# Optimization experiments

Hardware: AMD Instinct MI355X
Metric: run time of the kernel (lower is better)

Reference implementation:

```python
import jax, jax.numpy as jnp
import numpy as np
import math

N, C, T, V = 8, 256, 128, 25
H, HC = 8, 32            # num_heads, head_channels
W, DIL = 3, 1            # window, dilation
O = 256                  # out_channels
PAD = (W + (W - 1) * (DIL - 1) - 1) // 2
B, L = N * T, W * V


def _ln(x, g, b):
    m = jnp.mean(x, -1, keepdims=True)
    v = jnp.var(x, -1, keepdims=True)
    return (x - m) * jax.lax.rsqrt(v + 1e-5) * g + b


def setup_inputs() -> dict:
    key = jax.random.key(0)
    ks = iter(jax.random.split(key, 40))
    def w(shape):
        return jax.random.normal(next(ks), shape, jnp.float32) * 0.02
    d = {"x": jax.random.normal(next(ks), (N, C, T, V), jnp.float32)}
    d.update(
        ln1_g=jnp.ones((C,)), ln1_b=jnp.zeros((C,)),
        Wq=w((C, C)), bq=jnp.zeros((C,)), Wqa=w((C, H)), bqa=jnp.zeros((H,)),
        Wk=w((C, C)), bk=jnp.zeros((C,)), Wka=w((C, H)), bka=jnp.zeros((H,)),
        Wv=w((C, C)), bv=jnp.zeros((C,)), Wt=w((C, C)), bt=jnp.zeros((C,)),
        Wp=w((C, C)), bp=jnp.zeros((C,)),
        ffn_g=jnp.ones((C,)), ffn_b=jnp.zeros((C,)),
        W1=w((C, C)), b1=jnp.zeros((C,)), W2=w((C, C)), b2=jnp.zeros((C,)),
        tn_g=jnp.ones((C,)), tn_b=jnp.zeros((C,)),
        c1_w=w((C, O)), c1_b=jnp.zeros((O,)),
        c2_w=w((W, O, O)), c2_b=jnp.zeros((O,)),
    )
    return d


def reference(x, ln1_g, ln1_b, Wq, bq, Wqa, bqa, Wk, bk, Wka, bka, Wv, bv,
              Wt, bt, Wp, bp, ffn_g, ffn_b, W1, b1, W2, b2, tn_g, tn_b,
              c1_w, c1_b, c2_w, c2_b):
    scale = 1.0 / math.sqrt(HC)
    # ---- Unfold over time: build window of frames around each t (nn.Unfold) ----
    xp = jnp.pad(x, ((0, 0), (0, 0), (PAD, PAD), (0, 0)))
    win = jnp.stack([jax.lax.dynamic_slice_in_dim(xp, k * DIL, T, 2) for k in range(W)], 2)  # (N,C,W,T,V)
    seq = win.transpose(0, 3, 2, 4, 1).reshape(B, L, C)  # (N*T, W*V, C)

    sep = lambda z: z.reshape(B, L, H, HC).transpose(0, 2, 1, 3)  # (B,H,L,HC)
    grp = lambda z: z.transpose(0, 2, 1, 3).reshape(B, -1, C)

    # ---- SpatioTemporalAttention (eval: dropouts off) ----
    nx = _ln(seq, ln1_g, ln1_b)
    q = nx @ Wq + bq                                            # (B,L,C)
    qw = jax.nn.softmax((q @ Wqa + bqa).transpose(0, 2, 1) * scale, axis=-1)  # (B,H,L)
    pq = jnp.einsum('bhl,bhlc->bhc', qw, sep(q)).reshape(B, 1, C)             # pooled query
    keys = nx @ Wk + bk
    kw = jax.nn.softmax(((keys * pq) @ Wka + bka).transpose(0, 2, 1) * scale, axis=-1)
    pk = jnp.einsum('bhl,bhlc->bhc', kw, sep(keys))             # pooled key (B,H,HC)
    vals = sep(nx @ Wv + bv)
    kv = grp(vals * pk[:, :, None, :]) @ Wt + bt                # (B,L,C)
    attn = (kv + q) @ Wp + bp                                   # residual-in-heads == plain add

    # ---- AttentionBranch residual + FFN ----
    att = attn + seq
    f = _ln(att, ffn_g, ffn_b)
    y = jax.nn.gelu(f @ W1 + b1, approximate=False) @ W2 + b2 + att  # (B,L,C)

    # ---- temporal branch: LN -> regroup frames -> 1x1 conv -> GELU -> (W,1) conv stride W ----
    t5 = _ln(y, tn_g, tn_b).reshape(N, T, W, V, C)
    h = jax.nn.gelu(t5 @ c1_w + c1_b, approximate=False)        # (N,T,W,V,O)
    out = jnp.einsum('ntwvi,wio->ntvo', h, c2_w) + c2_b         # stride==kernel conv == window contraction
    return out.transpose(0, 3, 1, 2)                            # (N,O,T,V)
```

## Files before the change

### kernel.cpp

```cpp
#include <hip/hip_runtime.h>


#define DI __device__ __forceinline__

constexpr int CC   = 256;
constexpr int CL   = 75;
constexpr int CV   = 25;
constexpr int CT   = 128;
constexpr int TP   = 130;
constexpr int MPAD = 8 * TP * CV;
constexpr int MBL  = 1024 * CL;
constexpr int MOUT = 8 * CT * CV;
constexpr float SM_SCALE = 0.17677669529663687f;

typedef __bf16 bf16x8 __attribute__((ext_vector_type(8)));
typedef float f32x4 __attribute__((ext_vector_type(4)));

DI float bf2f(unsigned short u) { return __uint_as_float(((unsigned)u) << 16); }
DI float bf2f_lo(unsigned u) { return __uint_as_float(u << 16); }
DI float bf2f_hi(unsigned u) { return __uint_as_float(u & 0xffff0000u); }
DI unsigned short f2bf(float f) {
  unsigned u = __float_as_uint(f);
  u += 0x7fffu + ((u >> 16) & 1u);
  return (unsigned short)(u >> 16);
}
DI unsigned packbf(float a, float b) {
  return (unsigned)f2bf(a) | ((unsigned)f2bf(b) << 16);
}
DI float geluf(float x) { return 0.5f * x * (1.f + erff(x * 0.70710678118654752440f)); }

DI void gll16(const unsigned short* g, unsigned short* l) {
  __builtin_amdgcn_global_load_lds(
      (const __attribute__((address_space(1))) unsigned int*)g,
      (__attribute__((address_space(3))) unsigned int*)l, 16, 0, 0);
}

DI int arow(int r) {
  int b = r / CL;
  int l = r - b * CL;
  int w = l / CV;
  int v = l - w * CV;
  int t = b & (CT - 1);
  int n = b >> 7;
  return (n * TP + t + w) * CV + v;
}

__global__ __launch_bounds__(256) void k_transpose(const float* __restrict__ x,
                                                   unsigned short* __restrict__ xtp) {
  __shared__ float tile[32][33];
  const int n = blockIdx.z;
  const int c0 = blockIdx.x * 32;
  const int tv0 = blockIdx.y * 32;
  const int tx = threadIdx.x & 31, ty = threadIdx.x >> 5;
#pragma unroll
  for (int j = 0; j < 32; j += 8) {
    tile[ty + j][tx] = x[((size_t)(n * CC + c0 + ty + j)) * 3200 + tv0 + tx];
  }
  __syncthreads();
#pragma unroll
  for (int j = 0; j < 32; j += 8) {
    int tv = tv0 + ty + j;
    int st = tv / CV, v = tv - st * CV;
    size_t row = ((size_t)n * TP + st + 1) * CV + v;
    xtp[row * CC + c0 + tx] = f2bf(tile[tx][ty + j]);
  }
}

__global__ __launch_bounds__(256) void k_zero_pad(unsigned short* __restrict__ xtp) {
  int i = blockIdx.x * 256 + threadIdx.x;
  int c = i & 255;
  int rid = i >> 8;
  int n = rid / 50;
  int rem = rid - n * 50;
  int side = rem / 25;
  int v = rem - side * 25;
  size_t row = ((size_t)n * TP + side * (TP - 1)) * CV + v;
  xtp[row * CC + c] = 0;
}

struct TJobs {
  const float* src[10];
  unsigned short* dst[10];
  int stride[10];
  int off[10];
};
__global__ __launch_bounds__(256) void k_wtrans(TJobs J) {
  __shared__ float tile[32][33];
  const int j = blockIdx.z;
  const float* src = J.src[j];
  unsigned short* dst = J.dst[j];
  const int stride = J.stride[j], off = J.off[j];
  const int k0 = blockIdx.x * 32, n0 = blockIdx.y * 32;
  const int tx = threadIdx.x & 31, ty = threadIdx.x >> 5;
#pragma unroll
  for (int jj = 0; jj < 32; jj += 8)
    tile[ty + jj][tx] = src[(size_t)(k0 + ty + jj) * 256 + n0 + tx];
  __syncthreads();
#pragma unroll
  for (int jj = 0; jj < 32; jj += 8)
    dst[(size_t)(n0 + ty + jj) * stride + off + k0 + tx] = f2bf(tile[tx][ty + jj]);
}

__global__ __launch_bounds__(256) void k_wtwp(const float* __restrict__ Wt,
                                              const float* __restrict__ Wp,
                                              unsigned short* __restrict__ fused) {
  __shared__ float wrow[256];
  const int k = blockIdx.x, n = threadIdx.x;
  wrow[n] = Wt[(size_t)k * 256 + n];
  __syncthreads();
  float acc = 0.f;
  for (int j = 0; j < 256; ++j) acc = fmaf(wrow[j], Wp[(size_t)j * 256 + n], acc);
  fused[(size_t)n * 512 + k] = f2bf(acc);
}

__global__ __launch_bounds__(256) void k_bias2(const float* __restrict__ bt,
                                               const float* __restrict__ Wp,
                                               const float* __restrict__ bp,
                                               const float* __restrict__ bq,
                                               const float* __restrict__ bk,
                                               const float* __restrict__ bv,
                                               float* __restrict__ bias2,
                                               float* __restrict__ bias3) {
  const int n = threadIdx.x;
  float acc = bp[n];
  for (int j = 0; j < 256; ++j) acc = fmaf(bt[j], Wp[(size_t)j * 256 + n], acc);
  bias2[n] = acc;
  bias3[n] = bq[n];
  bias3[256 + n] = bk[n];
  bias3[512 + n] = bv[n];
}

__global__ __launch_bounds__(256) void k_ln4(const unsigned short* __restrict__ X,
                                             const float* __restrict__ g,
                                             const float* __restrict__ b,
                                             unsigned short* __restrict__ Y) {
  const int row = blockIdx.x * 4 + (threadIdx.x >> 6);
  const int lane = threadIdx.x & 63;
  const uint2 u = *(const uint2*)(X + (size_t)row * CC + lane * 4);
  const float x0 = bf2f_lo(u.x), x1 = bf2f_hi(u.x), x2 = bf2f_lo(u.y), x3 = bf2f_hi(u.y);
  float s = x0 + x1 + x2 + x3;
  float q = x0 * x0 + x1 * x1 + x2 * x2 + x3 * x3;
#pragma unroll
  for (int o = 32; o; o >>= 1) { s += __shfl_xor(s, o); q += __shfl_xor(q, o); }
  const float mean = s * (1.f / CC);
  const float var = q * (1.f / CC) - mean * mean;
  const float rs = rsqrtf(var + 1e-5f);
  const float4 g4 = *(const float4*)(g + lane * 4);
  const float4 b4 = *(const float4*)(b + lane * 4);
  uint2 o2;
  o2.x = packbf((x0 - mean) * rs * g4.x + b4.x, (x1 - mean) * rs * g4.y + b4.y);
  o2.y = packbf((x2 - mean) * rs * g4.z + b4.z, (x3 - mean) * rs * g4.w + b4.w);
  *(uint2*)(Y + (size_t)row * CC + lane * 4) = o2;
}

template <int AMODE, int EPI, int KD, bool MULTI>
__global__ __launch_bounds__(512) void k_mgemm(const unsigned short* __restrict__ A,
                                               const unsigned short* __restrict__ BwT,
                                               const float* __restrict__ bias,
                                               unsigned short* __restrict__ Cout,
                                               float* __restrict__ FOut,
                                               int M) {
  if constexpr (MULTI) {
    const int z = blockIdx.y;
    BwT += (size_t)z * (256 * 256);
    bias += z * 256;
    Cout += (size_t)z * MPAD * CC;
  }
  __shared__ unsigned short SH[20480];
  const int tid = threadIdx.x;
  const int lane = tid & 63;
  const int wid = tid >> 6;
  const int wm = wid >> 2, wn = wid & 3;
  const int r0 = blockIdx.x * 64;
  f32x4 acc[2][4] = {};

  const bool sa = tid < 256;
  const int rA = r0 + (tid >> 2);
  const int seg8 = (tid & 3) * 8;
  const bool valid = sa && (rA < M);
  int hrb = 0;
  if (valid && AMODE == 4) {
    const int nb = rA / 3200, rr = rA - nb * 3200;
    const int tq = rr / 25, vq = rr - tq * 25;
    hrb = (nb * CT + tq) * CL + vq;
  }

  auto loadA4 = [&](int k0) -> uint4 {
    uint4 u = make_uint4(0, 0, 0, 0);
    if (!valid) return u;
    const int w = k0 >> 8;
    u = *(const uint4*)(A + (size_t)(hrb + w * CV) * CC + (k0 & 255) + seg8);
    return u;
  };
  auto stageB = [&](int buf, int k0) {
    unsigned short* bs = SH + 4096 + buf * 8192;
#pragma unroll
    for (int pp = 0; pp < 2; ++pp) {
      const int s = tid + pp * 512;
      gll16(BwT + (size_t)(s >> 2) * KD + k0 + (s & 3) * 8, bs + s * 8);
    }
  };
  auto stageAg = [&](int buf, int k0) {
    if (valid) gll16(A + (size_t)rA * CC + k0 + seg8, SH + buf * 2048 + tid * 8);
  };

  stageB(0, 0);
  if constexpr (AMODE == 0) {
    stageAg(0, 0);
  } else {
    const uint4 a0 = loadA4(0);
    if (sa) *(uint4*)(SH + tid * 8) = a0;
  }
  __syncthreads();

  constexpr int NT = KD / 32;
  int cur = 0;
  for (int t = 0; t < NT; ++t) {
    const int nxt = cur ^ 1;
    const bool more = (t + 1 < NT);
    uint4 an;
    if (more) {
      stageB(nxt, (t + 1) * 32);
      if constexpr (AMODE == 0) stageAg(nxt, (t + 1) * 32);
      else an = loadA4((t + 1) * 32);
    }
    const unsigned short* as = SH + cur * 2048;
    const unsigned short* bs = SH + 4096 + cur * 8192;
    bf16x8 af[2], bfr[4];
#pragma unroll
    for (int mi = 0; mi < 2; ++mi)
      af[mi] = *(const bf16x8*)(as + (wm * 32 + mi * 16 + (lane & 15)) * 32 + (lane >> 4) * 8);
#pragma unroll
    for (int ni = 0; ni < 4; ++ni)
      bfr[ni] = *(const bf16x8*)(bs + (wn * 64 + ni * 16 + (lane & 15)) * 32 + (lane >> 4) * 8);
#pragma unroll
    for (int mi = 0; mi < 2; ++mi)
#pragma unroll
      for (int ni = 0; ni < 4; ++ni)
        acc[mi][ni] = __builtin_amdgcn_mfma_f32_16x16x32_bf16(af[mi], bfr[ni], acc[mi][ni], 0, 0, 0);
    if (more) {
      if constexpr (AMODE != 0) {
        if (sa) *(uint4*)(SH + nxt * 2048 + tid * 8) = an;
      }
      __syncthreads();
      cur = nxt;
    }
  }

  const int ln15 = lane & 15, lq = lane >> 4;
  if constexpr (EPI == 4) {
#pragma unroll
    for (int mi = 0; mi < 2; ++mi) {
#pragma unroll
      for (int ni = 0; ni < 4; ++ni) {
        const int col = wn * 64 + ni * 16 + ln15;
        const float bcol = bias[col];
        const int rbase = r0 + wm * 32 + mi * 16 + lq * 4;
        const int nb = rbase / 3200, rr = rbase - nb * 3200;
        float4 v;
        v.x = acc[mi][ni][0] + bcol;
        v.y = acc[mi][ni][1] + bcol;
        v.z = acc[mi][ni][2] + bcol;
        v.w = acc[mi][ni][3] + bcol;
        *(float4*)(FOut + (size_t)nb * 819200 + (size_t)col * 3200 + rr) = v;
      }
    }
  } else {
    constexpr int LDC = 260;
    __syncthreads();
#pragma unroll
    for (int mi = 0; mi < 2; ++mi) {
#pragma unroll
      for (int ni = 0; ni < 4; ++ni) {
        const int col = wn * 64 + ni * 16 + ln15;
        const float bcol = bias[col];
#pragma unroll
        for (int rg = 0; rg < 4; ++rg) {
          const int lrow = wm * 32 + mi * 16 + lq * 4 + rg;
          SH[lrow * LDC + col] = f2bf(acc[mi][ni][rg] + bcol);
        }
      }
    }
    __syncthreads();
#pragma unroll
    for (int i = 0; i < 4; ++i) {
      const int idx = tid + i * 512;
      const int row = idx >> 5, ch = idx & 31;
      const int gr = r0 + row;
      if (gr < M)
        *(uint4*)(Cout + (size_t)gr * CC + ch * 8) = *(const uint4*)&SH[row * LDC + ch * 8];
    }
  }
}

__global__ __launch_bounds__(512, 4) void k_chain(
    const unsigned short* __restrict__ VP, const unsigned short* __restrict__ QP,
    const float* __restrict__ PK, const unsigned short* __restrict__ XTP,
    const unsigned short* __restrict__ fusedB, const float* __restrict__ bias2,
    const unsigned short* __restrict__ W1T, const float* __restrict__ b1,
    const unsigned short* __restrict__ W2T, const float* __restrict__ b2,
    const float* __restrict__ ffn_g, const float* __restrict__ ffn_b,
    const unsigned short* __restrict__ c1wT, const float* __restrict__ c1b,
    const float* __restrict__ tn_g, const float* __restrict__ tn_b,
    unsigned short* __restrict__ Hout) {
  constexpr int LDC = 264;
  __shared__ unsigned short SH[16896 + 4096 + 16384];
  unsigned short* ACT = SH;
  unsigned short* AS = SH + 16896;
  unsigned short* BS = SH + 16896 + 4096;
  const int tid = threadIdx.x;
  const int lane = tid & 63, wid = tid >> 6;
  const int wm = wid >> 2, wn = wid & 3;
  const int ln15 = lane & 15, lq = lane >> 4;
  const int r0 = blockIdx.x * 64;

  const bool sa = tid < 256;
  const int rA = r0 + (tid >> 2);
  const int seg8 = (tid & 3) * 8;
  int ar = 0, bb = 0;
  if (sa) { ar = arow(rA); bb = rA / CL; }
  int xrow[8];
#pragma unroll
  for (int i = 0; i < 8; ++i)
    xrow[i] = arow(r0 + wm * 32 + (i >> 2) * 16 + lq * 4 + (i & 3));

  auto stageB = [&](const unsigned short* BwT, int KD, int buf, int k0) {
    unsigned short* bs = BS + buf * 8192;
#pragma unroll
    for (int pp = 0; pp < 2; ++pp) {
      const int s = tid + pp * 512;
      gll16(BwT + (size_t)(s >> 2) * KD + k0 + (s & 3) * 8, bs + s * 8);
    }
  };
  auto loadA5 = [&](int k0) -> uint4 {
    uint4 u = make_uint4(0, 0, 0, 0);
    if (!sa) return u;
    if (k0 < 256) {
      const int kg = k0 + seg8;
      const uint4 t4 = *(const uint4*)(VP + (size_t)ar * CC + kg);
      const float* sv = PK + bb * CC + kg;
      const float4 s0 = *(const float4*)sv;
      const float4 s1 = *(const float4*)(sv + 4);
      u.x = packbf(bf2f_lo(t4.x) * s0.x, bf2f_hi(t4.x) * s0.y);
      u.y = packbf(bf2f_lo(t4.y) * s0.z, bf2f_hi(t4.y) * s0.w);
      u.z = packbf(bf2f_lo(t4.z) * s1.x, bf2f_hi(t4.z) * s1.y);
      u.w = packbf(bf2f_lo(t4.w) * s1.z, bf2f_hi(t4.w) * s1.w);
    } else {
      u = *(const uint4*)(QP + (size_t)ar * CC + (k0 - 256) + seg8);
    }
    return u;
  };
  auto ln_inplace = [&](const float* g, const float* b) {
    const float4 g4 = *(const float4*)(g + lane * 4);
    const float4 b4 = *(const float4*)(b + lane * 4);
#pragma unroll
    for (int rr = 0; rr < 8; ++rr) {
      const int row = wid * 8 + rr;
      const uint2 u = *(const uint2*)(ACT + row * LDC + lane * 4);
      const float x0 = bf2f_lo(u.x), x1 = bf2f_hi(u.x);
      const float x2 = bf2f_lo(u.y), x3 = bf2f_hi(u.y);
      float s = x0 + x1 + x2 + x3;
      float q = x0 * x0 + x1 * x1 + x2 * x2 + x3 * x3;
#pragma unroll
      for (int o = 32; o; o >>= 1) { s += __shfl_xor(s, o); q += __shfl_xor(q, o); }
      const float mean = s * (1.f / CC);
      const float var = q * (1.f / CC) - mean * mean;
      const float rs = rsqrtf(var + 1e-5f);
      uint2 o2;
      o2.x = packbf((x0 - mean) * rs * g4.x + b4.x, (x1 - mean) * rs * g4.y + b4.y);
      o2.y = packbf((x2 - mean) * rs * g4.z + b4.z, (x3 - mean) * rs * g4.w + b4.w);
      *(uint2*)(ACT + row * LDC + lane * 4) = o2;
    }
  };
  auto gemmACT = [&](const unsigned short* BwT, f32x4 (&a)[2][4]) {
    int c2 = 0;
    for (int t = 0; t < 8; ++t) {
      if (t + 1 < 8) stageB(BwT, 256, c2 ^ 1, (t + 1) * 32);
      bf16x8 af[2], bfr[4];
#pragma unroll
      for (int mi = 0; mi < 2; ++mi)
        af[mi] = *(const bf16x8*)(ACT + (wm * 32 + mi * 16 + ln15) * LDC + t * 32 + lq * 8);
#pragma unroll
      for (int ni = 0; ni < 4; ++ni)
        bfr[ni] = *(const bf16x8*)(BS + c2 * 8192 + (wn * 64 + ni * 16 + ln15) * 32 + lq * 8);
#pragma unroll
      for (int mi = 0; mi < 2; ++mi)
#pragma unroll
        for (int ni = 0; ni < 4; ++ni)
          a[mi][ni] = __builtin_amdgcn_mfma_f32_16x16x32_bf16(af[mi], bfr[ni], a[mi][ni], 0, 0, 0);
      if (t + 1 < 8) { __syncthreads(); c2 ^= 1; }
    }
  };

  f32x4 acc[2][4] = {};
  stageB(fusedB, 512, 0, 0);
  { uint4 a0 = loadA5(0); if (sa) *(uint4*)(AS + tid * 8) = a0; }
  __syncthreads();
  int cur = 0;
  for (int t = 0; t < 16; ++t) {
    const int nxt = cur ^ 1;
    const bool more = (t + 1 < 16);
    uint4 an;
    if (more) { stageB(fusedB, 512, nxt, (t + 1) * 32); an = loadA5((t + 1) * 32); }
    bf16x8 af[2], bfr[4];
#pragma unroll
    for (int mi = 0; mi < 2; ++mi)
      af[mi] = *(const bf16x8*)(AS + cur * 2048 + (wm * 32 + mi * 16 + ln15) * 32 + lq * 8);
#pragma unroll
    for (int ni = 0; ni < 4; ++ni)
      bfr[ni] = *(const bf16x8*)(BS + cur * 8192 + (wn * 64 + ni * 16 + ln15) * 32 + lq * 8);
#pragma unroll
    for (int mi = 0; mi < 2; ++mi)
#pragma unroll
      for (int ni = 0; ni < 4; ++ni)
        acc[mi][ni] = __builtin_amdgcn_mfma_f32_16x16x32_bf16(af[mi], bfr[ni], acc[mi][ni], 0, 0, 0);
    if (more) {
      if (sa) *(uint4*)(AS + nxt * 2048 + tid * 8) = an;
      __syncthreads();
      cur = nxt;
    }
  }
  stageB(W1T, 256, 0, 0);
  f32x4 attres[2][4];
#pragma unroll
  for (int mi = 0; mi < 2; ++mi) {
#pragma unroll
    for (int ni = 0; ni < 4; ++ni) {
      const int col = wn * 64 + ni * 16 + ln15;
      const float bcol = bias2[col];
#pragma unroll
      for (int rg = 0; rg < 4; ++rg) {
        attres[mi][ni][rg] =
            acc[mi][ni][rg] + bcol + bf2f(XTP[(size_t)xrow[mi * 4 + rg] * CC + col]);
        ACT[(wm * 32 + mi * 16 + lq * 4 + rg) * LDC + col] = f2bf(attres[mi][ni][rg]);
      }
    }
  }
  __syncthreads();
  ln_inplace(ffn_g, ffn_b);
  __syncthreads();

  f32x4 acc2[2][4] = {};
  gemmACT(W1T, acc2);
  stageB(W2T, 256, 0, 0);
  __syncthreads();
#pragma unroll
  for (int mi = 0; mi < 2; ++mi)
#pragma unroll
    for (int ni = 0; ni < 4; ++ni) {
      const int col = wn * 64 + ni * 16 + ln15;
      const float bcol = b1[col];
#pragma unroll
      for (int rg = 0; rg < 4; ++rg)
        ACT[(wm * 32 + mi * 16 + lq * 4 + rg) * LDC + col] = f2bf(geluf(acc2[mi][ni][rg] + bcol));
    }
  __syncthreads();

  f32x4 acc3[2][4] = {};
  gemmACT(W2T, acc3);
  stageB(c1wT, 256, 0, 0);
  __syncthreads();
#pragma unroll
  for (int mi = 0; mi < 2; ++mi)
#pragma unroll
    for (int ni = 0; ni < 4; ++ni) {
      const int col = wn * 64 + ni * 16 + ln15;
      const float bcol = b2[col];
#pragma unroll
      for (int rg = 0; rg < 4; ++rg)
        ACT[(wm * 32 + mi * 16 + lq * 4 + rg) * LDC + col] =
            f2bf(acc3[mi][ni][rg] + bcol + attres[mi][ni][rg]);
    }
  __syncthreads();
  ln_inplace(tn_g, tn_b);
  __syncthreads();

  f32x4 acc4[2][4] = {};
  gemmACT(c1wT, acc4);
  __syncthreads();
#pragma unroll
  for (int mi = 0; mi < 2; ++mi)
#pragma unroll
    for (int ni = 0; ni < 4; ++ni) {
      const int col = wn * 64 + ni * 16 + ln15;
      const float bcol = c1b[col];
#pragma unroll
      for (int rg = 0; rg < 4; ++rg)
        ACT[(wm * 32 + mi * 16 + lq * 4 + rg) * LDC + col] = f2bf(geluf(acc4[mi][ni][rg] + bcol));
    }
  __syncthreads();
#pragma unroll
  for (int i = 0; i < 4; ++i) {
    const int idx = tid + i * 512;
    const int row = idx >> 5, ch = idx & 31;
    *(uint4*)(Hout + (size_t)(r0 + row) * CC + ch * 8) = *(const uint4*)&ACT[row * LDC + ch * 8];
  }
}

template <int SIDE>
__global__ __launch_bounds__(256) void k_attpool(const unsigned short* __restrict__ ROWS,
                                                 const float* __restrict__ PQ,
                                                 const float* __restrict__ W8,
                                                 const float* __restrict__ b8,
                                                 float* __restrict__ OUT) {
  __shared__ unsigned short rows[CL * CC];
  __shared__ float uu[8 * 258];
  __shared__ float lg[8 * 76];
  __shared__ float inv8[8];
  __shared__ int arl[CL];
  const int b = blockIdx.x;
  const int t = threadIdx.x;

  if (t < CL) arl[t] = arow(b * CL + t);
  __syncthreads();

  for (int i = t; i < CL * 32; i += 256) {
    const int r = i >> 5, seg = i & 31;
    gll16(ROWS + (size_t)arl[r] * CC + seg * 8, &rows[i * 8]);
  }
  for (int i = t; i < CC * 8; i += 256) {
    const int c = i >> 3, h = i & 7;
    if constexpr (SIDE == 0)
      uu[h * 258 + c] = W8[c * 8 + h];
    else
      uu[h * 258 + c] = PQ[(size_t)b * CC + c] * W8[c * 8 + h];
  }
  __syncthreads();

  {
    const int c0 = (t & 127) * 2;
    for (int i = t; i < CL * 8; i += 256) {
      const int h = i / CL, l = i - h * CL;
      float acc = b8[h];
#pragma unroll 4
      for (int jj = 0; jj < CC; jj += 2) {
        const int c = (c0 + jj) & 255;
        const unsigned pr = *(const unsigned*)&rows[l * CC + c];
        acc = fmaf(bf2f_lo(pr), uu[h * 258 + c], acc);
        acc = fmaf(bf2f_hi(pr), uu[h * 258 + c + 1], acc);
      }
      lg[h * 76 + l] = acc * SM_SCALE;
    }
  }
  __syncthreads();

  if (t < 8) {
    float m = -1e30f;
    for (int l = 0; l < CL; ++l) m = fmaxf(m, lg[t * 76 + l]);
    float s = 0.f;
    for (int l = 0; l < CL; ++l) {
      const float e = __expf(lg[t * 76 + l] - m);
      lg[t * 76 + l] = e;
      s += e;
    }
    inv8[t] = 1.f / s;
  }
  __syncthreads();

  {
    const int h = t >> 5;
    float acc = 0.f;
    for (int l = 0; l < CL; ++l) acc = fmaf(lg[h * 76 + l], bf2f(rows[l * CC + t]), acc);
    OUT[(size_t)b * CC + t] = acc * inv8[h];
  }
}

extern "C" void kernel_launch(void* const* d_in, const int* in_sizes, int n_in,
                              void* d_out, int out_size, void* d_ws, size_t ws_size,
                              hipStream_t stream) {
  const float* x = (const float*)d_in[0];
  const float* ln1_g = (const float*)d_in[1];
  const float* ln1_b = (const float*)d_in[2];
  const float* Wq = (const float*)d_in[3];
  const float* bq = (const float*)d_in[4];
  const float* Wqa = (const float*)d_in[5];
  const float* bqa = (const float*)d_in[6];
  const float* Wk = (const float*)d_in[7];
  const float* bk = (const float*)d_in[8];
  const float* Wka = (const float*)d_in[9];
  const float* bka = (const float*)d_in[10];
  const float* Wv = (const float*)d_in[11];
  const float* bv = (const float*)d_in[12];
  const float* Wt = (const float*)d_in[13];
  const float* bt = (const float*)d_in[14];
  const float* Wp = (const float*)d_in[15];
  const float* bp = (const float*)d_in[16];
  const float* ffn_g = (const float*)d_in[17];
  const float* ffn_b = (const float*)d_in[18];
  const float* W1 = (const float*)d_in[19];
  const float* b1 = (const float*)d_in[20];
  const float* W2 = (const float*)d_in[21];
  const float* b2 = (const float*)d_in[22];
  const float* tn_g = (const float*)d_in[23];
  const float* tn_b = (const float*)d_in[24];
  const float* c1w = (const float*)d_in[25];
  const float* c1b = (const float*)d_in[26];
  const float* c2w = (const float*)d_in[27];
  const float* c2b = (const float*)d_in[28];
  float* out = (float*)d_out;

  char* wp = (char*)d_ws;
  auto alloc = [&](size_t bytes) -> char* {
    char* p = wp;
    wp += (bytes + 255) & ~(size_t)255;
    return p;
  };
  unsigned short* XTP = (unsigned short*)alloc((size_t)MPAD * CC * 2);
  unsigned short* LNXP = (unsigned short*)alloc((size_t)MPAD * CC * 2);
  unsigned short* QKVP = (unsigned short*)alloc((size_t)3 * MPAD * CC * 2);
  unsigned short* QP = QKVP;
  unsigned short* KP = QKVP + (size_t)MPAD * CC;
  unsigned short* VP = QKVP + (size_t)2 * MPAD * CC;
  unsigned short* Hb = (unsigned short*)alloc((size_t)MBL * CC * 2);
  float* PQ = (float*)alloc((size_t)1024 * CC * 4);
  float* PK = (float*)alloc((size_t)1024 * CC * 4);
  unsigned short* WqkvT = (unsigned short*)alloc((size_t)3 * 256 * 256 * 2);
  unsigned short* W1T = (unsigned short*)alloc(256 * 256 * 2);
  unsigned short* W2T = (unsigned short*)alloc(256 * 256 * 2);
  unsigned short* c1wT = (unsigned short*)alloc(256 * 256 * 2);
  unsigned short* c2wT = (unsigned short*)alloc(256 * 768 * 2);
  unsigned short* fusedB = (unsigned short*)alloc(256 * 512 * 2);
  float* bias2 = (float*)alloc(256 * 4);
  float* bias3 = (float*)alloc(768 * 4);

  TJobs J;
  const float* srcs[10] = {Wq, Wk, Wv, W1, W2, c1w, c2w, c2w + 65536, c2w + 131072, Wp};
  unsigned short* dsts[10] = {WqkvT, WqkvT + 65536, WqkvT + 131072, W1T, W2T, c1wT,
                              c2wT, c2wT, c2wT, fusedB};
  const int strides[10] = {256, 256, 256, 256, 256, 256, 768, 768, 768, 512};
  const int offs[10] = {0, 0, 0, 0, 0, 0, 0, 256, 512, 256};
  for (int i = 0; i < 10; ++i) {
    J.src[i] = srcs[i]; J.dst[i] = dsts[i]; J.stride[i] = strides[i]; J.off[i] = offs[i];
  }
  k_wtrans<<<dim3(8, 8, 10), 256, 0, stream>>>(J);
  k_wtwp<<<256, 256, 0, stream>>>(Wt, Wp, fusedB);
  k_bias2<<<1, 256, 0, stream>>>(bt, Wp, bp, bq, bk, bv, bias2, bias3);

  k_transpose<<<dim3(8, 100, 8), 256, 0, stream>>>(x, XTP);
  k_zero_pad<<<400, 256, 0, stream>>>(XTP);
  k_ln4<<<MPAD / 4, 256, 0, stream>>>(XTP, ln1_g, ln1_b, LNXP);

  const int gP = (MPAD + 63) / 64;
  const int gO = MOUT / 64;
  k_mgemm<0, 0, 256, true><<<dim3(gP, 3), 512, 0, stream>>>(
      LNXP, WqkvT, bias3, QKVP, nullptr, MPAD);

  k_attpool<0><<<1024, 256, 0, stream>>>(QP, nullptr, Wqa, bqa, PQ);
  k_attpool<1><<<1024, 256, 0, stream>>>(KP, PQ, Wka, bka, PK);

  k_chain<<<MBL / 64, 512, 0, stream>>>(VP, QP, PK, XTP, fusedB, bias2,
                                        W1T, b1, W2T, b2, ffn_g, ffn_b,
                                        c1wT, c1b, tn_g, tn_b, Hb);

  k_mgemm<4, 4, 768, false><<<gO, 512, 0, stream>>>(Hb, c2wT, c2b, nullptr, out, MOUT);
}
```

Baseline: 311.7 us.

## Replace syncthreads with vmcnt-counted waits and raw barriers in GEMM k-loops

Rewrites the double-buffered k-loops of the generic GEMM (AMODE 0 path) and the fused gemmACT stages to use explicit s_waitcnt vmcnt counts on the async global-to-LDS loads plus raw s_barrier calls instead of __syncthreads. The aim is to let the next tile's loads stay in flight while the current tile is consumed, instead of draining all memory ops at every barrier. Out-of-range A rows are clamped so every thread issues the same number of async loads, which keeps the vmcnt counts uniform. The initial B staging moves inside gemmACT, so it no longer overlaps with the preceding epilogue. The hand-set wait counts are fragile and depend on exactly how many loads each wave issues.

```diff
diff --git a/kernel.cpp b/kernel.cpp
--- a/kernel.cpp
+++ b/kernel.cpp
@@ -176,10 +176,10 @@
 
   const bool sa = tid < 256;
   const int rA = r0 + (tid >> 2);
+  const int rAc = (rA < M) ? rA : (M - 1);
   const int seg8 = (tid & 3) * 8;
-  const bool valid = sa && (rA < M);
   int hrb = 0;
-  if (valid && AMODE == 4) {
+  if (sa && AMODE == 4 && rA < M) {
     const int nb = rA / 3200, rr = rA - nb * 3200;
     const int tq = rr / 25, vq = rr - tq * 25;
     hrb = (nb * CT + tq) * CL + vq;
@@ -187,7 +187,7 @@
 
   auto loadA4 = [&](int k0) -> uint4 {
     uint4 u = make_uint4(0, 0, 0, 0);
-    if (!valid) return u;
+    if (!(sa && rA < M)) return u;
     const int w = k0 >> 8;
     u = *(const uint4*)(A + (size_t)(hrb + w * CV) * CC + (k0 & 255) + seg8);
     return u;
@@ -201,29 +201,9 @@
     }
   };
   auto stageAg = [&](int buf, int k0) {
-    if (valid) gll16(A + (size_t)rA * CC + k0 + seg8, SH + buf * 2048 + tid * 8);
-  };
-
-  stageB(0, 0);
-  if constexpr (AMODE == 0) {
-    stageAg(0, 0);
-  } else {
-    const uint4 a0 = loadA4(0);
-    if (sa) *(uint4*)(SH + tid * 8) = a0;
-  }
-  __syncthreads();
-
-  constexpr int NT = KD / 32;
-  int cur = 0;
-  for (int t = 0; t < NT; ++t) {
-    const int nxt = cur ^ 1;
-    const bool more = (t + 1 < NT);
-    uint4 an;
-    if (more) {
-      stageB(nxt, (t + 1) * 32);
-      if constexpr (AMODE == 0) stageAg(nxt, (t + 1) * 32);
-      else an = loadA4((t + 1) * 32);
-    }
+    if (sa) gll16(A + (size_t)rAc * CC + k0 + seg8, SH + buf * 2048 + tid * 8);
+  };
+  auto mfmaStep = [&](int cur) {
     const unsigned short* as = SH + cur * 2048;
     const unsigned short* bs = SH + 4096 + cur * 8192;
     bf16x8 af[2], bfr[4];
@@ -238,12 +218,51 @@
 #pragma unroll
       for (int ni = 0; ni < 4; ++ni)
         acc[mi][ni] = __builtin_amdgcn_mfma_f32_16x16x32_bf16(af[mi], bfr[ni], acc[mi][ni], 0, 0, 0);
-    if (more) {
-      if constexpr (AMODE != 0) {
+  };
+
+  constexpr int NT = KD / 32;
+  if constexpr (AMODE == 0) {
+    asm volatile("s_waitcnt vmcnt(0)" ::: "memory");
+    stageB(0, 0);
+    stageAg(0, 0);
+    for (int t = 0; t < NT; ++t) {
+      const int cur = t & 1;
+      const bool more = (t + 1 < NT);
+      if (more) { stageB(cur ^ 1, (t + 1) * 32); stageAg(cur ^ 1, (t + 1) * 32); }
+      if (wid < 4) {
+        if (more) asm volatile("s_waitcnt vmcnt(3)" ::: "memory");
+        else      asm volatile("s_waitcnt vmcnt(0)" ::: "memory");
+      } else {
+        if (more) asm volatile("s_waitcnt vmcnt(2)" ::: "memory");
+        else      asm volatile("s_waitcnt vmcnt(0)" ::: "memory");
+      }
+      __builtin_amdgcn_s_barrier();
+      asm volatile("" ::: "memory");
+      mfmaStep(cur);
+      asm volatile("s_waitcnt lgkmcnt(0)" ::: "memory");
+      __builtin_amdgcn_s_barrier();
+      asm volatile("" ::: "memory");
+    }
+    __syncthreads();
+  } else {
+    stageB(0, 0);
+    {
+      const uint4 a0 = loadA4(0);
+      if (sa) *(uint4*)(SH + tid * 8) = a0;
+    }
+    __syncthreads();
+    int cur = 0;
+    for (int t = 0; t < NT; ++t) {
+      const int nxt = cur ^ 1;
+      const bool more = (t + 1 < NT);
+      uint4 an;
+      if (more) { stageB(nxt, (t + 1) * 32); an = loadA4((t + 1) * 32); }
+      mfmaStep(cur);
+      if (more) {
         if (sa) *(uint4*)(SH + nxt * 2048 + tid * 8) = an;
+        __syncthreads();
+        cur = nxt;
       }
-      __syncthreads();
-      cur = nxt;
     }
   }
 
@@ -267,7 +286,7 @@
     }
   } else {
     constexpr int LDC = 260;
-    __syncthreads();
+    if constexpr (AMODE != 0) __syncthreads();
 #pragma unroll
     for (int mi = 0; mi < 2; ++mi) {
 #pragma unroll
@@ -373,22 +392,31 @@
     }
   };
   auto gemmACT = [&](const unsigned short* BwT, f32x4 (&a)[2][4]) {
-    int c2 = 0;
+    asm volatile("s_waitcnt vmcnt(0)" ::: "memory");
+    stageB(BwT, 256, 0, 0);
     for (int t = 0; t < 8; ++t) {
-      if (t + 1 < 8) stageB(BwT, 256, c2 ^ 1, (t + 1) * 32);
+      const int cur = t & 1;
+      const bool more = (t + 1 < 8);
+      if (more) stageB(BwT, 256, cur ^ 1, (t + 1) * 32);
+      if (more) asm volatile("s_waitcnt vmcnt(2)" ::: "memory");
+      else      asm volatile("s_waitcnt vmcnt(0)" ::: "memory");
+      __builtin_amdgcn_s_barrier();
+      asm volatile("" ::: "memory");
       bf16x8 af[2], bfr[4];
 #pragma unroll
       for (int mi = 0; mi < 2; ++mi)
         af[mi] = *(const bf16x8*)(ACT + (wm * 32 + mi * 16 + ln15) * LDC + t * 32 + lq * 8);
 #pragma unroll
       for (int ni = 0; ni < 4; ++ni)
-        bfr[ni] = *(const bf16x8*)(BS + c2 * 8192 + (wn * 64 + ni * 16 + ln15) * 32 + lq * 8);
+        bfr[ni] = *(const bf16x8*)(BS + cur * 8192 + (wn * 64 + ni * 16 + ln15) * 32 + lq * 8);
 #pragma unroll
       for (int mi = 0; mi < 2; ++mi)
 #pragma unroll
         for (int ni = 0; ni < 4; ++ni)
           a[mi][ni] = __builtin_amdgcn_mfma_f32_16x16x32_bf16(af[mi], bfr[ni], a[mi][ni], 0, 0, 0);
-      if (t + 1 < 8) { __syncthreads(); c2 ^= 1; }
+      asm volatile("s_waitcnt lgkmcnt(0)" ::: "memory");
+      __builtin_amdgcn_s_barrier();
+      asm volatile("" ::: "memory");
     }
   };
 
@@ -420,7 +448,6 @@
       cur = nxt;
     }
   }
-  stageB(W1T, 256, 0, 0);
   f32x4 attres[2][4];
 #pragma unroll
   for (int mi = 0; mi < 2; ++mi) {
@@ -442,7 +469,6 @@
 
   f32x4 acc2[2][4] = {};
   gemmACT(W1T, acc2);
-  stageB(W2T, 256, 0, 0);
   __syncthreads();
 #pragma unroll
   for (int mi = 0; mi < 2; ++mi)
@@ -458,7 +484,6 @@
 
   f32x4 acc3[2][4] = {};
   gemmACT(W2T, acc3);
-  stageB(c1wT, 256, 0, 0);
   __syncthreads();
 #pragma unroll
   for (int mi = 0; mi < 2; ++mi)
```

Result: faster. 305.3 us (-2.1%).
